# Kernel tuning notes

Hardware: AMD Instinct MI355X
Metric: run time of the kernel (lower is better)

The kernel has to match this reference:

```python
import jax, jax.numpy as jnp
import numpy as np

D_QK = 32  # out_channels // 8


def conv1x1(x, w, b):
    # x: [B,C,H,W], w: [O,C], b: [O] -> [B,O,H,W]
    return jnp.einsum('bchw,oc->bohw', x, w) + b[None, :, None, None]


def setup_inputs() -> dict:
    key = jax.random.key(0)
    ks = jax.random.split(key, 10)
    B, C, H, W = 4, 256, 64, 64
    in_ch, out_ch, attn_ch = 512, 256, 256
    s_in = 1.0 / np.sqrt(in_ch)
    s_at = 1.0 / np.sqrt(attn_ch)
    return {
        'ef': jax.random.normal(ks[0], (B, C, H, W), jnp.float32),
        'sf': jax.random.normal(ks[1], (B, C, H, W), jnp.float32),
        'Attn': jax.random.normal(ks[2], (B, attn_ch, H, W), jnp.float32),
        'Qw': jax.random.uniform(ks[3], (D_QK, in_ch), jnp.float32, -s_in, s_in),
        'Qb': jax.random.uniform(ks[4], (D_QK,), jnp.float32, -s_in, s_in),
        'Kw': jax.random.uniform(ks[5], (D_QK, attn_ch), jnp.float32, -s_at, s_at),
        'Kb': jax.random.uniform(ks[6], (D_QK,), jnp.float32, -s_at, s_at),
        'Vw': jax.random.uniform(ks[7], (out_ch, in_ch), jnp.float32, -s_in, s_in),
        'Vb': jax.random.uniform(ks[8], (out_ch,), jnp.float32, -s_in, s_in),
        'gamma': jnp.ones((1,), jnp.float32) * 0.25,
    }


def reference(ef, sf, Attn, Qw, Qb, Kw, Kb, Vw, Vb, gamma):
    B, C, H, W = ef.shape
    N = H * W
    x = jnp.concatenate((ef, sf), axis=1)  # [B, 2C, H, W]
    q = conv1x1(x, Qw, Qb).reshape(B, D_QK, N)         # [B, d, N]
    k = conv1x1(Attn, Kw, Kb).reshape(B, D_QK, N)      # [B, d, N]
    # scores[b, m, n] = sum_d q[b, d, m] * k[b, d, n]  (no 1/sqrt(d) scale)
    scores = jnp.einsum('bdm,bdn->bmn', q, k)
    attn = jax.nn.softmax(scores, axis=-1)             # [B, N, N]
    v = conv1x1(x, Vw, Vb).reshape(B, C, N)            # [B, C, N]
    # out[b, c, m] = sum_n v[b, c, n] * attn[b, m, n]
    out = jnp.einsum('bcn,bmn->bcm', v, attn).reshape(B, C, H, W)
    return gamma[0] * out + ef
```

## Files before the change

kernel.cpp:

```cpp
#include <hip/hip_runtime.h>
#include <hip/hip_bf16.h>

typedef short bf16x8 __attribute__((ext_vector_type(8)));
typedef float f32x4 __attribute__((ext_vector_type(4)));

#define MFMA16(a, b, c) __builtin_amdgcn_mfma_f32_16x16x32_bf16(a, b, c, 0, 0, 0)

#define NB 4
#define NC 256
#define NSP 4096

__device__ __forceinline__ unsigned short f2bf(float f) {
    return (unsigned short)((__float_as_uint(f) + 0x8000u) >> 16);
}
__device__ __forceinline__ unsigned pk2bf(float hi, float lo) {
    return __builtin_amdgcn_perm(__float_as_uint(hi) + 0x8000u,
                                 __float_as_uint(lo) + 0x8000u, 0x07060302u);
}

__global__ __launch_bounds__(256) void prep_w(
    const float* __restrict__ Qw, const float* __restrict__ Kw,
    const float* __restrict__ Vw,
    unsigned short* __restrict__ Qwbf, unsigned short* __restrict__ Kwbf,
    unsigned short* __restrict__ Vwbf)
{
    int i = blockIdx.x * 256 + threadIdx.x;
    {
        const float4* vs = (const float4*)(Vw + (size_t)i * 8);
        float4 a = vs[0], c = vs[1];
        int4 st;
        st.x = (int)pk2bf(a.y, a.x); st.y = (int)pk2bf(a.w, a.z);
        st.z = (int)pk2bf(c.y, c.x); st.w = (int)pk2bf(c.w, c.z);
        *(int4*)(Vwbf + (size_t)i * 8) = st;
    }
    if (i < 2048) {
        const float4* qs = (const float4*)(Qw + (size_t)i * 8);
        float4 a = qs[0], c = qs[1];
        int4 st;
        st.x = (int)pk2bf(a.y, a.x); st.y = (int)pk2bf(a.w, a.z);
        st.z = (int)pk2bf(c.y, c.x); st.w = (int)pk2bf(c.w, c.z);
        *(int4*)(Qwbf + (size_t)i * 8) = st;
    }
    if (i < 1024) {
        const float4* ks = (const float4*)(Kw + (size_t)i * 8);
        float4 a = ks[0], c = ks[1];
        int4 st;
        st.x = (int)pk2bf(a.y, a.x); st.y = (int)pk2bf(a.w, a.z);
        st.z = (int)pk2bf(c.y, c.x); st.w = (int)pk2bf(c.w, c.z);
        *(int4*)(Kwbf + (size_t)i * 8) = st;
    }
}

__global__ __launch_bounds__(256) void prep_x(
    const float* __restrict__ ef, const float* __restrict__ sf,
    const float* __restrict__ attn,
    unsigned short* __restrict__ xt, unsigned short* __restrict__ at)
{
    __shared__ float tile[64][65];
    int gid = blockIdx.x;
    const float* src; unsigned short* dst;
    int mt, cdst0, CW;
    if (gid < 2048) {
        int b = gid >> 9, r = gid & 511;
        mt = r >> 3; int ct = r & 7;
        src = (ct < 4 ? ef : sf) + ((size_t)(b * NC) + (ct & 3) * 64) * NSP;
        dst = xt + (size_t)b * NSP * 512; cdst0 = ct * 64; CW = 512;
    } else {
        int g2 = gid - 2048;
        int b = g2 >> 8, r = g2 & 255;
        mt = r >> 2; int ct = r & 3;
        src = attn + ((size_t)(b * NC) + ct * 64) * NSP;
        dst = at + (size_t)b * NSP * 256; cdst0 = ct * 64; CW = 256;
    }
    int m0 = mt * 64;
    int t = threadIdx.x;
    int ml = t & 63, cl = t >> 6;
#pragma unroll
    for (int r = 0; r < 16; ++r)
        tile[ml][r * 4 + cl] = src[(size_t)(r * 4 + cl) * NSP + m0 + ml];
    __syncthreads();
    int cp = t & 31, mw = t >> 5;
#pragma unroll
    for (int r = 0; r < 8; ++r) {
        int m_l = r * 8 + mw;
        float v0 = tile[m_l][2 * cp], v1 = tile[m_l][2 * cp + 1];
        *(unsigned*)(dst + (size_t)(m0 + m_l) * CW + cdst0 + 2 * cp) = pk2bf(v1, v0);
    }
}

__global__ __launch_bounds__(256) void proj_qk(
    const unsigned short* __restrict__ xt, const unsigned short* __restrict__ at,
    const unsigned short* __restrict__ Qwbf, const unsigned short* __restrict__ Kwbf,
    const float* __restrict__ Qb, const float* __restrict__ Kb,
    unsigned short* __restrict__ qws, unsigned short* __restrict__ kws)
{
    int t = threadIdx.x;
    int w = t >> 6, lane = t & 63, quad = lane >> 4, l15 = lane & 15;
    int b = blockIdx.x >> 6, m0 = (blockIdx.x & 63) * 64;
    int m = m0 + w * 16;

    f32x4 zero = {0.f, 0.f, 0.f, 0.f};
    f32x4 aq0 = zero, aq1 = zero, ak0 = zero, ak1 = zero;

    const unsigned short* xrow = xt + ((size_t)(b * NSP) + m + l15) * 512;
#pragma unroll
    for (int ks = 0; ks < 16; ++ks) {
        bf16x8 af = *(const bf16x8*)(xrow + ks * 32 + quad * 8);
        bf16x8 b0 = *(const bf16x8*)(Qwbf + (size_t)l15 * 512 + ks * 32 + quad * 8);
        bf16x8 b1 = *(const bf16x8*)(Qwbf + (size_t)(16 + l15) * 512 + ks * 32 + quad * 8);
        aq0 = MFMA16(af, b0, aq0);
        aq1 = MFMA16(af, b1, aq1);
    }
    const unsigned short* arow = at + ((size_t)(b * NSP) + m + l15) * 256;
#pragma unroll
    for (int ks = 0; ks < 8; ++ks) {
        bf16x8 af = *(const bf16x8*)(arow + ks * 32 + quad * 8);
        bf16x8 b0 = *(const bf16x8*)(Kwbf + (size_t)l15 * 256 + ks * 32 + quad * 8);
        bf16x8 b1 = *(const bf16x8*)(Kwbf + (size_t)(16 + l15) * 256 + ks * 32 + quad * 8);
        ak0 = MFMA16(af, b0, ak0);
        ak1 = MFMA16(af, b1, ak1);
    }
    float bq0 = Qb[l15], bq1 = Qb[16 + l15];
    float bk0 = Kb[l15], bk1 = Kb[16 + l15];
#pragma unroll
    for (int r = 0; r < 4; ++r) {
        size_t mr = (size_t)(b * NSP) + m + quad * 4 + r;
        qws[mr * 32 + l15]      = f2bf(aq0[r] + bq0);
        qws[mr * 32 + 16 + l15] = f2bf(aq1[r] + bq1);
        kws[mr * 32 + l15]      = f2bf(ak0[r] + bk0);
        kws[mr * 32 + 16 + l15] = f2bf(ak1[r] + bk1);
    }
}

__global__ __launch_bounds__(256) void proj_v(
    const unsigned short* __restrict__ xt,
    const unsigned short* __restrict__ Vwbf, const float* __restrict__ Vb,
    unsigned short* __restrict__ vws)
{
    int t = threadIdx.x;
    int w = t >> 6, lane = t & 63, quad = lane >> 4, l15 = lane & 15;
    int mt = blockIdx.x, coh = blockIdx.y, b = blockIdx.z;
    int m0 = mt * 32;
    int co0 = coh * 128 + w * 32;

    f32x4 zero = {0.f, 0.f, 0.f, 0.f};
    f32x4 acc[2][2];
    acc[0][0] = zero; acc[0][1] = zero; acc[1][0] = zero; acc[1][1] = zero;

    const unsigned short* x0 = xt + ((size_t)(b * NSP) + m0 + l15) * 512;
    const unsigned short* x1 = x0 + 16 * 512;
    const unsigned short* vw0 = Vwbf + (size_t)(co0 + l15) * 512;
    const unsigned short* vw1 = Vwbf + (size_t)(co0 + 16 + l15) * 512;
#pragma unroll
    for (int ks = 0; ks < 16; ++ks) {
        bf16x8 a0 = *(const bf16x8*)(x0 + ks * 32 + quad * 8);
        bf16x8 a1 = *(const bf16x8*)(x1 + ks * 32 + quad * 8);
        bf16x8 b0 = *(const bf16x8*)(vw0 + ks * 32 + quad * 8);
        bf16x8 b1 = *(const bf16x8*)(vw1 + ks * 32 + quad * 8);
        acc[0][0] = MFMA16(a0, b0, acc[0][0]);
        acc[0][1] = MFMA16(a0, b1, acc[0][1]);
        acc[1][0] = MFMA16(a1, b0, acc[1][0]);
        acc[1][1] = MFMA16(a1, b1, acc[1][1]);
    }
#pragma unroll
    for (int mi = 0; mi < 2; ++mi)
#pragma unroll
        for (int ci = 0; ci < 2; ++ci) {
            int co = co0 + ci * 16 + l15;
            float bias = Vb[co];
            unsigned short* vp = vws + ((size_t)(b * 128 + mt) * 256 + co) * 32;
#pragma unroll
            for (int r = 0; r < 4; ++r)
                vp[2 * (quad * 4 + r) + mi] = f2bf(acc[mi][ci][r] + bias);
        }
}

__global__ __launch_bounds__(512, 2) void attention(
    const unsigned short* __restrict__ qws, const unsigned short* __restrict__ kws,
    const unsigned short* __restrict__ vws, const float* __restrict__ ef,
    const float* __restrict__ gamma, float* __restrict__ out)
{
    __shared__ unsigned short Plds[2][2][64 * 40];
    __shared__ float mrg[256][68];
    __shared__ float denl[2][64];

    int t = threadIdx.x;
    int g = t >> 8, tl = t & 255;
    int w = tl >> 6, lane = tl & 63, quad = lane >> 4, l15 = lane & 15;
    int b = blockIdx.x >> 6, m0 = (blockIdx.x & 63) << 6;

    const unsigned short* kbase = kws + (size_t)(b * NSP) * 32;
    const unsigned short* vbase = vws + (size_t)(b * 128) * 8192;

    bf16x8 qf = *(const bf16x8*)(qws + ((size_t)(b * NSP) + m0 + w * 16 + l15) * 32 + quad * 8);

    f32x4 zero = {0.f, 0.f, 0.f, 0.f};
    f32x4 acc[4][4];
#pragma unroll
    for (int i = 0; i < 4; ++i)
#pragma unroll
        for (int j = 0; j < 4; ++j) acc[i][j] = zero;
    float lp0 = 0.f, lp1 = 0.f, lp2 = 0.f, lp3 = 0.f;

    int nt0 = g * 64;
    bf16x8 kf0 = *(const bf16x8*)(kbase + (size_t)(nt0 * 32 + l15) * 32 + quad * 8);
    bf16x8 kf1 = *(const bf16x8*)(kbase + (size_t)(nt0 * 32 + 16 + l15) * 32 + quad * 8);
    bf16x8 vf[4];
#pragma unroll
    for (int cc = 0; cc < 4; ++cc)
        vf[cc] = *(const bf16x8*)(vbase + (size_t)nt0 * 8192 + (w * 64 + cc * 16 + l15) * 32 + quad * 8);

    for (int it = 0; it < 64; ++it) {
        int buf = it & 1;
        f32x4 s0 = MFMA16(qf, kf0, zero);
        f32x4 s1 = MFMA16(qf, kf1, zero);
        float e00 = __expf(s0[0]), e01 = __expf(s0[1]), e02 = __expf(s0[2]), e03 = __expf(s0[3]);
        float e10 = __expf(s1[0]), e11 = __expf(s1[1]), e12 = __expf(s1[2]), e13 = __expf(s1[3]);
        lp0 += e00 + e10; lp1 += e01 + e11; lp2 += e02 + e12; lp3 += e03 + e13;

        {
            unsigned short* pb = &Plds[g][buf][(w * 16 + quad * 4) * 40 + 2 * l15];
            *(unsigned*)(pb)           = pk2bf(e10, e00);
            *(unsigned*)(pb + 40)      = pk2bf(e11, e01);
            *(unsigned*)(pb + 80)      = pk2bf(e12, e02);
            *(unsigned*)(pb + 120)     = pk2bf(e13, e03);
        }

        int itn = it + 1 < 64 ? it + 1 : 63;
        int ntn = nt0 + itn;
        kf0 = *(const bf16x8*)(kbase + (size_t)(ntn * 32 + l15) * 32 + quad * 8);
        kf1 = *(const bf16x8*)(kbase + (size_t)(ntn * 32 + 16 + l15) * 32 + quad * 8);
        bf16x8 vfn[4];
#pragma unroll
        for (int cc = 0; cc < 4; ++cc)
            vfn[cc] = *(const bf16x8*)(vbase + (size_t)ntn * 8192 + (w * 64 + cc * 16 + l15) * 32 + quad * 8);

        __syncthreads();

        bf16x8 pa0 = *(const bf16x8*)&Plds[g][buf][(0  + l15) * 40 + quad * 8];
        bf16x8 pa1 = *(const bf16x8*)&Plds[g][buf][(16 + l15) * 40 + quad * 8];
        bf16x8 pa2 = *(const bf16x8*)&Plds[g][buf][(32 + l15) * 40 + quad * 8];
        bf16x8 pa3 = *(const bf16x8*)&Plds[g][buf][(48 + l15) * 40 + quad * 8];
#pragma unroll
        for (int cc = 0; cc < 4; ++cc) {
            acc[0][cc] = MFMA16(pa0, vf[cc], acc[0][cc]);
            acc[1][cc] = MFMA16(pa1, vf[cc], acc[1][cc]);
            acc[2][cc] = MFMA16(pa2, vf[cc], acc[2][cc]);
            acc[3][cc] = MFMA16(pa3, vf[cc], acc[3][cc]);
        }
#pragma unroll
        for (int cc = 0; cc < 4; ++cc) vf[cc] = vfn[cc];
    }

    lp0 += __shfl_xor(lp0, 1); lp0 += __shfl_xor(lp0, 2); lp0 += __shfl_xor(lp0, 4); lp0 += __shfl_xor(lp0, 8);
    lp1 += __shfl_xor(lp1, 1); lp1 += __shfl_xor(lp1, 2); lp1 += __shfl_xor(lp1, 4); lp1 += __shfl_xor(lp1, 8);
    lp2 += __shfl_xor(lp2, 1); lp2 += __shfl_xor(lp2, 2); lp2 += __shfl_xor(lp2, 4); lp2 += __shfl_xor(lp2, 8);
    lp3 += __shfl_xor(lp3, 1); lp3 += __shfl_xor(lp3, 2); lp3 += __shfl_xor(lp3, 4); lp3 += __shfl_xor(lp3, 8);
    if (l15 == 0) {
        int base = w * 16 + quad * 4;
        denl[g][base + 0] = lp0; denl[g][base + 1] = lp1;
        denl[g][base + 2] = lp2; denl[g][base + 3] = lp3;
    }
    if (g == 1) {
#pragma unroll
        for (int qc = 0; qc < 4; ++qc)
#pragma unroll
            for (int cc = 0; cc < 4; ++cc)
                *(f32x4*)&mrg[w * 64 + cc * 16 + l15][qc * 16 + quad * 4] = acc[qc][cc];
    }
    __syncthreads();

    if (g == 0) {
        float gam = gamma[0];
#pragma unroll
        for (int qc = 0; qc < 4; ++qc) {
            int qb = qc * 16 + quad * 4;
            float4 d0 = *(const float4*)&denl[0][qb];
            float4 d1 = *(const float4*)&denl[1][qb];
            float r0 = gam / (d0.x + d1.x), r1 = gam / (d0.y + d1.y);
            float r2 = gam / (d0.z + d1.z), r3 = gam / (d0.w + d1.w);
#pragma unroll
            for (int cc = 0; cc < 4; ++cc) {
                int ch = w * 64 + cc * 16 + l15;
                f32x4 part = *(const f32x4*)&mrg[ch][qb];
                size_t off = ((size_t)(b * NC + ch)) * NSP + m0 + qb;
                float4 e = *(const float4*)(ef + off);
                float4 o;
                o.x = (acc[qc][cc][0] + part[0]) * r0 + e.x;
                o.y = (acc[qc][cc][1] + part[1]) * r1 + e.y;
                o.z = (acc[qc][cc][2] + part[2]) * r2 + e.z;
                o.w = (acc[qc][cc][3] + part[3]) * r3 + e.w;
                *(float4*)(out + off) = o;
            }
        }
    }
}

extern "C" void kernel_launch(void* const* d_in, const int* in_sizes, int n_in,
                              void* d_out, int out_size, void* d_ws, size_t ws_size,
                              hipStream_t stream) {
    const float* ef    = (const float*)d_in[0];
    const float* sf    = (const float*)d_in[1];
    const float* attn  = (const float*)d_in[2];
    const float* Qw    = (const float*)d_in[3];
    const float* Qb    = (const float*)d_in[4];
    const float* Kw    = (const float*)d_in[5];
    const float* Kb    = (const float*)d_in[6];
    const float* Vw    = (const float*)d_in[7];
    const float* Vb    = (const float*)d_in[8];
    const float* gamma = (const float*)d_in[9];
    float* out = (float*)d_out;

    unsigned short* qws  = (unsigned short*)d_ws;
    unsigned short* kws  = qws + (size_t)4 * 4096 * 32;
    unsigned short* vws  = kws + (size_t)4 * 4096 * 32;
    unsigned short* xt   = vws + (size_t)4 * 128 * 256 * 32;
    unsigned short* at   = xt  + (size_t)4 * 4096 * 512;
    unsigned short* Qwbf = at  + (size_t)4 * 4096 * 256;
    unsigned short* Kwbf = Qwbf + 32 * 512;
    unsigned short* Vwbf = Kwbf + 32 * 256;

    hipLaunchKernelGGL(prep_w, dim3(64), dim3(256), 0, stream,
                       Qw, Kw, Vw, Qwbf, Kwbf, Vwbf);
    hipLaunchKernelGGL(prep_x, dim3(3072), dim3(256), 0, stream,
                       ef, sf, attn, xt, at);
    hipLaunchKernelGGL(proj_qk, dim3(256), dim3(256), 0, stream,
                       xt, at, Qwbf, Kwbf, Qb, Kb, qws, kws);
    hipLaunchKernelGGL(proj_v, dim3(128, 2, 4), dim3(256), 0, stream,
                       xt, Vwbf, Vb, vws);
    hipLaunchKernelGGL(attention, dim3(256), dim3(512), 0, stream,
                       qws, kws, vws, ef, gamma, out);
}
```

Measured before the change: 202.4 us.

## Merge prep/projection kernels, fold log2e into Q, process two key tiles per step

Merges the weight and activation prep kernels into one launch, and the Q/K/V projections into a single launch, which cuts kernel-launch overhead and the gaps between kernels. Q is prescaled by log2(e) so the attention loop can call the hardware exp2 directly instead of __expf. The attention inner loop now handles two 32-key tiles per iteration, with a wider LDS P buffer, so it does half as many barriers and more MFMAs per sync. The cost is higher register pressure from double K/V prefetch fragments, and the extra bf16 rounding of the scaled Q can shift accuracy slightly.

```diff
diff --git a/kernel.cpp b/kernel.cpp
--- a/kernel.cpp
+++ b/kernel.cpp
@@ -9,6 +9,7 @@
 #define NB 4
 #define NC 256
 #define NSP 4096
+#define LOG2E 1.4426950408889634f
 
 __device__ __forceinline__ unsigned short f2bf(float f) {
     return (unsigned short)((__float_as_uint(f) + 0x8000u) >> 16);
@@ -18,46 +19,48 @@
                                  __float_as_uint(lo) + 0x8000u, 0x07060302u);
 }
 
-__global__ __launch_bounds__(256) void prep_w(
+__global__ __launch_bounds__(256) void prep(
+    const float* __restrict__ ef, const float* __restrict__ sf,
+    const float* __restrict__ attn,
     const float* __restrict__ Qw, const float* __restrict__ Kw,
     const float* __restrict__ Vw,
+    unsigned short* __restrict__ xt, unsigned short* __restrict__ at,
     unsigned short* __restrict__ Qwbf, unsigned short* __restrict__ Kwbf,
     unsigned short* __restrict__ Vwbf)
 {
-    int i = blockIdx.x * 256 + threadIdx.x;
-    {
-        const float4* vs = (const float4*)(Vw + (size_t)i * 8);
-        float4 a = vs[0], c = vs[1];
-        int4 st;
-        st.x = (int)pk2bf(a.y, a.x); st.y = (int)pk2bf(a.w, a.z);
-        st.z = (int)pk2bf(c.y, c.x); st.w = (int)pk2bf(c.w, c.z);
-        *(int4*)(Vwbf + (size_t)i * 8) = st;
-    }
-    if (i < 2048) {
-        const float4* qs = (const float4*)(Qw + (size_t)i * 8);
-        float4 a = qs[0], c = qs[1];
-        int4 st;
-        st.x = (int)pk2bf(a.y, a.x); st.y = (int)pk2bf(a.w, a.z);
-        st.z = (int)pk2bf(c.y, c.x); st.w = (int)pk2bf(c.w, c.z);
-        *(int4*)(Qwbf + (size_t)i * 8) = st;
-    }
-    if (i < 1024) {
-        const float4* ks = (const float4*)(Kw + (size_t)i * 8);
-        float4 a = ks[0], c = ks[1];
-        int4 st;
-        st.x = (int)pk2bf(a.y, a.x); st.y = (int)pk2bf(a.w, a.z);
-        st.z = (int)pk2bf(c.y, c.x); st.w = (int)pk2bf(c.w, c.z);
-        *(int4*)(Kwbf + (size_t)i * 8) = st;
-    }
-}
-
-__global__ __launch_bounds__(256) void prep_x(
-    const float* __restrict__ ef, const float* __restrict__ sf,
-    const float* __restrict__ attn,
-    unsigned short* __restrict__ xt, unsigned short* __restrict__ at)
-{
     __shared__ float tile[64][65];
     int gid = blockIdx.x;
+    int t = threadIdx.x;
+
+    if (gid >= 3072) {
+        int i = (gid - 3072) * 256 + t;
+        {
+            const float4* vs = (const float4*)(Vw + (size_t)i * 8);
+            float4 a = vs[0], c = vs[1];
+            int4 st;
+            st.x = (int)pk2bf(a.y, a.x); st.y = (int)pk2bf(a.w, a.z);
+            st.z = (int)pk2bf(c.y, c.x); st.w = (int)pk2bf(c.w, c.z);
+            *(int4*)(Vwbf + (size_t)i * 8) = st;
+        }
+        if (i < 2048) {
+            const float4* qs = (const float4*)(Qw + (size_t)i * 8);
+            float4 a = qs[0], c = qs[1];
+            int4 st;
+            st.x = (int)pk2bf(a.y, a.x); st.y = (int)pk2bf(a.w, a.z);
+            st.z = (int)pk2bf(c.y, c.x); st.w = (int)pk2bf(c.w, c.z);
+            *(int4*)(Qwbf + (size_t)i * 8) = st;
+        }
+        if (i < 1024) {
+            const float4* ks = (const float4*)(Kw + (size_t)i * 8);
+            float4 a = ks[0], c = ks[1];
+            int4 st;
+            st.x = (int)pk2bf(a.y, a.x); st.y = (int)pk2bf(a.w, a.z);
+            st.z = (int)pk2bf(c.y, c.x); st.w = (int)pk2bf(c.w, c.z);
+            *(int4*)(Kwbf + (size_t)i * 8) = st;
+        }
+        return;
+    }
+
     const float* src; unsigned short* dst;
     int mt, cdst0, CW;
     if (gid < 2048) {
@@ -73,7 +76,6 @@
         dst = at + (size_t)b * NSP * 256; cdst0 = ct * 64; CW = 256;
     }
     int m0 = mt * 64;
-    int t = threadIdx.x;
     int ml = t & 63, cl = t >> 6;
 #pragma unroll
     for (int r = 0; r < 16; ++r)
@@ -88,91 +90,95 @@
     }
 }
 
-__global__ __launch_bounds__(256) void proj_qk(
+__global__ __launch_bounds__(256, 4) void proj(
     const unsigned short* __restrict__ xt, const unsigned short* __restrict__ at,
     const unsigned short* __restrict__ Qwbf, const unsigned short* __restrict__ Kwbf,
+    const unsigned short* __restrict__ Vwbf,
     const float* __restrict__ Qb, const float* __restrict__ Kb,
-    unsigned short* __restrict__ qws, unsigned short* __restrict__ kws)
+    const float* __restrict__ Vb,
+    unsigned short* __restrict__ qws, unsigned short* __restrict__ kws,
+    unsigned short* __restrict__ vws)
 {
+    int bi = blockIdx.x;
     int t = threadIdx.x;
     int w = t >> 6, lane = t & 63, quad = lane >> 4, l15 = lane & 15;
-    int b = blockIdx.x >> 6, m0 = (blockIdx.x & 63) * 64;
-    int m = m0 + w * 16;
-
     f32x4 zero = {0.f, 0.f, 0.f, 0.f};
-    f32x4 aq0 = zero, aq1 = zero, ak0 = zero, ak1 = zero;
-
-    const unsigned short* xrow = xt + ((size_t)(b * NSP) + m + l15) * 512;
-#pragma unroll
-    for (int ks = 0; ks < 16; ++ks) {
-        bf16x8 af = *(const bf16x8*)(xrow + ks * 32 + quad * 8);
-        bf16x8 b0 = *(const bf16x8*)(Qwbf + (size_t)l15 * 512 + ks * 32 + quad * 8);
-        bf16x8 b1 = *(const bf16x8*)(Qwbf + (size_t)(16 + l15) * 512 + ks * 32 + quad * 8);
-        aq0 = MFMA16(af, b0, aq0);
-        aq1 = MFMA16(af, b1, aq1);
-    }
-    const unsigned short* arow = at + ((size_t)(b * NSP) + m + l15) * 256;
-#pragma unroll
-    for (int ks = 0; ks < 8; ++ks) {
-        bf16x8 af = *(const bf16x8*)(arow + ks * 32 + quad * 8);
-        bf16x8 b0 = *(const bf16x8*)(Kwbf + (size_t)l15 * 256 + ks * 32 + quad * 8);
-        bf16x8 b1 = *(const bf16x8*)(Kwbf + (size_t)(16 + l15) * 256 + ks * 32 + quad * 8);
-        ak0 = MFMA16(af, b0, ak0);
-        ak1 = MFMA16(af, b1, ak1);
-    }
-    float bq0 = Qb[l15], bq1 = Qb[16 + l15];
-    float bk0 = Kb[l15], bk1 = Kb[16 + l15];
-#pragma unroll
-    for (int r = 0; r < 4; ++r) {
-        size_t mr = (size_t)(b * NSP) + m + quad * 4 + r;
-        qws[mr * 32 + l15]      = f2bf(aq0[r] + bq0);
-        qws[mr * 32 + 16 + l15] = f2bf(aq1[r] + bq1);
-        kws[mr * 32 + l15]      = f2bf(ak0[r] + bk0);
-        kws[mr * 32 + 16 + l15] = f2bf(ak1[r] + bk1);
-    }
-}
-
-__global__ __launch_bounds__(256) void proj_v(
-    const unsigned short* __restrict__ xt,
-    const unsigned short* __restrict__ Vwbf, const float* __restrict__ Vb,
-    unsigned short* __restrict__ vws)
-{
-    int t = threadIdx.x;
-    int w = t >> 6, lane = t & 63, quad = lane >> 4, l15 = lane & 15;
-    int mt = blockIdx.x, coh = blockIdx.y, b = blockIdx.z;
-    int m0 = mt * 32;
-    int co0 = coh * 128 + w * 32;
-
-    f32x4 zero = {0.f, 0.f, 0.f, 0.f};
-    f32x4 acc[2][2];
-    acc[0][0] = zero; acc[0][1] = zero; acc[1][0] = zero; acc[1][1] = zero;
-
-    const unsigned short* x0 = xt + ((size_t)(b * NSP) + m0 + l15) * 512;
-    const unsigned short* x1 = x0 + 16 * 512;
-    const unsigned short* vw0 = Vwbf + (size_t)(co0 + l15) * 512;
-    const unsigned short* vw1 = Vwbf + (size_t)(co0 + 16 + l15) * 512;
-#pragma unroll
-    for (int ks = 0; ks < 16; ++ks) {
-        bf16x8 a0 = *(const bf16x8*)(x0 + ks * 32 + quad * 8);
-        bf16x8 a1 = *(const bf16x8*)(x1 + ks * 32 + quad * 8);
-        bf16x8 b0 = *(const bf16x8*)(vw0 + ks * 32 + quad * 8);
-        bf16x8 b1 = *(const bf16x8*)(vw1 + ks * 32 + quad * 8);
-        acc[0][0] = MFMA16(a0, b0, acc[0][0]);
-        acc[0][1] = MFMA16(a0, b1, acc[0][1]);
-        acc[1][0] = MFMA16(a1, b0, acc[1][0]);
-        acc[1][1] = MFMA16(a1, b1, acc[1][1]);
-    }
-#pragma unroll
-    for (int mi = 0; mi < 2; ++mi)
-#pragma unroll
-        for (int ci = 0; ci < 2; ++ci) {
-            int co = co0 + ci * 16 + l15;
-            float bias = Vb[co];
-            unsigned short* vp = vws + ((size_t)(b * 128 + mt) * 256 + co) * 32;
-#pragma unroll
-            for (int r = 0; r < 4; ++r)
-                vp[2 * (quad * 4 + r) + mi] = f2bf(acc[mi][ci][r] + bias);
-        }
+
+    if (bi < 256) {
+        int b = bi >> 6, m = (bi & 63) * 64 + w * 16;
+        f32x4 a0 = zero, a1 = zero;
+        const unsigned short* xrow = xt + ((size_t)(b * NSP) + m + l15) * 512;
+#pragma unroll 4
+        for (int ks = 0; ks < 16; ++ks) {
+            bf16x8 af = *(const bf16x8*)(xrow + ks * 32 + quad * 8);
+            bf16x8 b0 = *(const bf16x8*)(Qwbf + (size_t)l15 * 512 + ks * 32 + quad * 8);
+            bf16x8 b1 = *(const bf16x8*)(Qwbf + (size_t)(16 + l15) * 512 + ks * 32 + quad * 8);
+            a0 = MFMA16(af, b0, a0);
+            a1 = MFMA16(af, b1, a1);
+        }
+        float bq0 = Qb[l15], bq1 = Qb[16 + l15];
+#pragma unroll
+        for (int r = 0; r < 4; ++r) {
+            size_t mr = (size_t)(b * NSP) + m + quad * 4 + r;
+            qws[mr * 32 + l15]      = f2bf((a0[r] + bq0) * LOG2E);
+            qws[mr * 32 + 16 + l15] = f2bf((a1[r] + bq1) * LOG2E);
+        }
+    } else if (bi < 512) {
+        int r2 = bi - 256;
+        int b = r2 >> 6, m = (r2 & 63) * 64 + w * 16;
+        f32x4 a0 = zero, a1 = zero;
+        const unsigned short* arow = at + ((size_t)(b * NSP) + m + l15) * 256;
+#pragma unroll 4
+        for (int ks = 0; ks < 8; ++ks) {
+            bf16x8 af = *(const bf16x8*)(arow + ks * 32 + quad * 8);
+            bf16x8 b0 = *(const bf16x8*)(Kwbf + (size_t)l15 * 256 + ks * 32 + quad * 8);
+            bf16x8 b1 = *(const bf16x8*)(Kwbf + (size_t)(16 + l15) * 256 + ks * 32 + quad * 8);
+            a0 = MFMA16(af, b0, a0);
+            a1 = MFMA16(af, b1, a1);
+        }
+        float bk0 = Kb[l15], bk1 = Kb[16 + l15];
+#pragma unroll
+        for (int r = 0; r < 4; ++r) {
+            size_t mr = (size_t)(b * NSP) + m + quad * 4 + r;
+            kws[mr * 32 + l15]      = f2bf(a0[r] + bk0);
+            kws[mr * 32 + 16 + l15] = f2bf(a1[r] + bk1);
+        }
+    } else {
+        int r2 = bi - 512;
+        int mt = r2 & 127, coh = (r2 >> 7) & 1, b = r2 >> 8;
+        int m0 = mt * 32;
+        int co0 = coh * 128 + w * 32;
+
+        f32x4 acc[2][2];
+        acc[0][0] = zero; acc[0][1] = zero; acc[1][0] = zero; acc[1][1] = zero;
+
+        const unsigned short* x0 = xt + ((size_t)(b * NSP) + m0 + l15) * 512;
+        const unsigned short* x1 = x0 + 16 * 512;
+        const unsigned short* vw0 = Vwbf + (size_t)(co0 + l15) * 512;
+        const unsigned short* vw1 = Vwbf + (size_t)(co0 + 16 + l15) * 512;
+#pragma unroll 4
+        for (int ks = 0; ks < 16; ++ks) {
+            bf16x8 a0 = *(const bf16x8*)(x0 + ks * 32 + quad * 8);
+            bf16x8 a1 = *(const bf16x8*)(x1 + ks * 32 + quad * 8);
+            bf16x8 b0 = *(const bf16x8*)(vw0 + ks * 32 + quad * 8);
+            bf16x8 b1 = *(const bf16x8*)(vw1 + ks * 32 + quad * 8);
+            acc[0][0] = MFMA16(a0, b0, acc[0][0]);
+            acc[0][1] = MFMA16(a0, b1, acc[0][1]);
+            acc[1][0] = MFMA16(a1, b0, acc[1][0]);
+            acc[1][1] = MFMA16(a1, b1, acc[1][1]);
+        }
+#pragma unroll
+        for (int mi = 0; mi < 2; ++mi)
+#pragma unroll
+            for (int ci = 0; ci < 2; ++ci) {
+                int co = co0 + ci * 16 + l15;
+                float bias = Vb[co];
+                unsigned short* vp = vws + ((size_t)(b * 128 + mt) * 256 + co) * 32;
+#pragma unroll
+                for (int r = 0; r < 4; ++r)
+                    vp[2 * (quad * 4 + r) + mi] = f2bf(acc[mi][ci][r] + bias);
+            }
+    }
 }
 
 __global__ __launch_bounds__(512, 2) void attention(
@@ -180,7 +186,7 @@
     const unsigned short* __restrict__ vws, const float* __restrict__ ef,
     const float* __restrict__ gamma, float* __restrict__ out)
 {
-    __shared__ unsigned short Plds[2][2][64 * 40];
+    __shared__ unsigned short Plds[2][2][64 * 72];
     __shared__ float mrg[256][68];
     __shared__ float denl[2][64];
 
@@ -202,54 +208,77 @@
         for (int j = 0; j < 4; ++j) acc[i][j] = zero;
     float lp0 = 0.f, lp1 = 0.f, lp2 = 0.f, lp3 = 0.f;
 
-    int nt0 = g * 64;
-    bf16x8 kf0 = *(const bf16x8*)(kbase + (size_t)(nt0 * 32 + l15) * 32 + quad * 8);
-    bf16x8 kf1 = *(const bf16x8*)(kbase + (size_t)(nt0 * 32 + 16 + l15) * 32 + quad * 8);
-    bf16x8 vf[4];
-#pragma unroll
-    for (int cc = 0; cc < 4; ++cc)
-        vf[cc] = *(const bf16x8*)(vbase + (size_t)nt0 * 8192 + (w * 64 + cc * 16 + l15) * 32 + quad * 8);
-
-    for (int it = 0; it < 64; ++it) {
+    int tt0 = g * 64;
+    bf16x8 kf[4];
+#pragma unroll
+    for (int j = 0; j < 4; ++j)
+        kf[j] = *(const bf16x8*)(kbase + (size_t)((tt0 + (j >> 1)) * 32 + (j & 1) * 16 + l15) * 32 + quad * 8);
+    bf16x8 vf[2][4];
+#pragma unroll
+    for (int h = 0; h < 2; ++h)
+#pragma unroll
+        for (int cc = 0; cc < 4; ++cc)
+            vf[h][cc] = *(const bf16x8*)(vbase + (size_t)(tt0 + h) * 8192 + (w * 64 + cc * 16 + l15) * 32 + quad * 8);
+
+    for (int it = 0; it < 32; ++it) {
         int buf = it & 1;
-        f32x4 s0 = MFMA16(qf, kf0, zero);
-        f32x4 s1 = MFMA16(qf, kf1, zero);
-        float e00 = __expf(s0[0]), e01 = __expf(s0[1]), e02 = __expf(s0[2]), e03 = __expf(s0[3]);
-        float e10 = __expf(s1[0]), e11 = __expf(s1[1]), e12 = __expf(s1[2]), e13 = __expf(s1[3]);
-        lp0 += e00 + e10; lp1 += e01 + e11; lp2 += e02 + e12; lp3 += e03 + e13;
-
-        {
-            unsigned short* pb = &Plds[g][buf][(w * 16 + quad * 4) * 40 + 2 * l15];
-            *(unsigned*)(pb)           = pk2bf(e10, e00);
-            *(unsigned*)(pb + 40)      = pk2bf(e11, e01);
-            *(unsigned*)(pb + 80)      = pk2bf(e12, e02);
-            *(unsigned*)(pb + 120)     = pk2bf(e13, e03);
-        }
-
-        int itn = it + 1 < 64 ? it + 1 : 63;
-        int ntn = nt0 + itn;
-        kf0 = *(const bf16x8*)(kbase + (size_t)(ntn * 32 + l15) * 32 + quad * 8);
-        kf1 = *(const bf16x8*)(kbase + (size_t)(ntn * 32 + 16 + l15) * 32 + quad * 8);
-        bf16x8 vfn[4];
-#pragma unroll
-        for (int cc = 0; cc < 4; ++cc)
-            vfn[cc] = *(const bf16x8*)(vbase + (size_t)ntn * 8192 + (w * 64 + cc * 16 + l15) * 32 + quad * 8);
+        f32x4 s0 = MFMA16(qf, kf[0], zero);
+        f32x4 s1 = MFMA16(qf, kf[1], zero);
+        f32x4 s2 = MFMA16(qf, kf[2], zero);
+        f32x4 s3 = MFMA16(qf, kf[3], zero);
+
+        float e0[4], e1[4], e2[4], e3[4];
+#pragma unroll
+        for (int r = 0; r < 4; ++r) {
+            e0[r] = __builtin_amdgcn_exp2f(s0[r]);
+            e1[r] = __builtin_amdgcn_exp2f(s1[r]);
+            e2[r] = __builtin_amdgcn_exp2f(s2[r]);
+            e3[r] = __builtin_amdgcn_exp2f(s3[r]);
+        }
+        lp0 += (e0[0] + e1[0]) + (e2[0] + e3[0]);
+        lp1 += (e0[1] + e1[1]) + (e2[1] + e3[1]);
+        lp2 += (e0[2] + e1[2]) + (e2[2] + e3[2]);
+        lp3 += (e0[3] + e1[3]) + (e2[3] + e3[3]);
+
+        unsigned short* pd = &Plds[g][buf][(w * 16 + quad * 4) * 72 + 2 * l15];
+#pragma unroll
+        for (int r = 0; r < 4; ++r) {
+            *(unsigned*)(pd + r * 72)      = pk2bf(e1[r], e0[r]);
+            *(unsigned*)(pd + r * 72 + 32) = pk2bf(e3[r], e2[r]);
+        }
+
+        int itn = it + 1 < 32 ? it + 1 : 31;
+        int ttn = tt0 + 2 * itn;
+#pragma unroll
+        for (int j = 0; j < 4; ++j)
+            kf[j] = *(const bf16x8*)(kbase + (size_t)((ttn + (j >> 1)) * 32 + (j & 1) * 16 + l15) * 32 + quad * 8);
+        bf16x8 vfn[2][4];
+#pragma unroll
+        for (int h = 0; h < 2; ++h)
+#pragma unroll
+            for (int cc = 0; cc < 4; ++cc)
+                vfn[h][cc] = *(const bf16x8*)(vbase + (size_t)(ttn + h) * 8192 + (w * 64 + cc * 16 + l15) * 32 + quad * 8);
 
         __syncthreads();
 
-        bf16x8 pa0 = *(const bf16x8*)&Plds[g][buf][(0  + l15) * 40 + quad * 8];
-        bf16x8 pa1 = *(const bf16x8*)&Plds[g][buf][(16 + l15) * 40 + quad * 8];
-        bf16x8 pa2 = *(const bf16x8*)&Plds[g][buf][(32 + l15) * 40 + quad * 8];
-        bf16x8 pa3 = *(const bf16x8*)&Plds[g][buf][(48 + l15) * 40 + quad * 8];
-#pragma unroll
-        for (int cc = 0; cc < 4; ++cc) {
-            acc[0][cc] = MFMA16(pa0, vf[cc], acc[0][cc]);
-            acc[1][cc] = MFMA16(pa1, vf[cc], acc[1][cc]);
-            acc[2][cc] = MFMA16(pa2, vf[cc], acc[2][cc]);
-            acc[3][cc] = MFMA16(pa3, vf[cc], acc[3][cc]);
-        }
-#pragma unroll
-        for (int cc = 0; cc < 4; ++cc) vf[cc] = vfn[cc];
+#pragma unroll
+        for (int h = 0; h < 2; ++h) {
+            bf16x8 pa0 = *(const bf16x8*)&Plds[g][buf][(0  + l15) * 72 + h * 32 + quad * 8];
+            bf16x8 pa1 = *(const bf16x8*)&Plds[g][buf][(16 + l15) * 72 + h * 32 + quad * 8];
+            bf16x8 pa2 = *(const bf16x8*)&Plds[g][buf][(32 + l15) * 72 + h * 32 + quad * 8];
+            bf16x8 pa3 = *(const bf16x8*)&Plds[g][buf][(48 + l15) * 72 + h * 32 + quad * 8];
+#pragma unroll
+            for (int cc = 0; cc < 4; ++cc) {
+                acc[0][cc] = MFMA16(pa0, vf[h][cc], acc[0][cc]);
+                acc[1][cc] = MFMA16(pa1, vf[h][cc], acc[1][cc]);
+                acc[2][cc] = MFMA16(pa2, vf[h][cc], acc[2][cc]);
+                acc[3][cc] = MFMA16(pa3, vf[h][cc], acc[3][cc]);
+            }
+        }
+#pragma unroll
+        for (int h = 0; h < 2; ++h)
+#pragma unroll
+            for (int cc = 0; cc < 4; ++cc) vf[h][cc] = vfn[h][cc];
     }
 
     lp0 += __shfl_xor(lp0, 1); lp0 += __shfl_xor(lp0, 2); lp0 += __shfl_xor(lp0, 4); lp0 += __shfl_xor(lp0, 8);
@@ -320,14 +349,10 @@
     unsigned short* Kwbf = Qwbf + 32 * 512;
     unsigned short* Vwbf = Kwbf + 32 * 256;
 
-    hipLaunchKernelGGL(prep_w, dim3(64), dim3(256), 0, stream,
-                       Qw, Kw, Vw, Qwbf, Kwbf, Vwbf);
-    hipLaunchKernelGGL(prep_x, dim3(3072), dim3(256), 0, stream,
-                       ef, sf, attn, xt, at);
-    hipLaunchKernelGGL(proj_qk, dim3(256), dim3(256), 0, stream,
-                       xt, at, Qwbf, Kwbf, Qb, Kb, qws, kws);
-    hipLaunchKernelGGL(proj_v, dim3(128, 2, 4), dim3(256), 0, stream,
-                       xt, Vwbf, Vb, vws);
+    hipLaunchKernelGGL(prep, dim3(3136), dim3(256), 0, stream,
+                       ef, sf, attn, Qw, Kw, Vw, xt, at, Qwbf, Kwbf, Vwbf);
+    hipLaunchKernelGGL(proj, dim3(1536), dim3(256), 0, stream,
+                       xt, at, Qwbf, Kwbf, Vwbf, Qb, Kb, Vb, qws, kws, vws);
     hipLaunchKernelGGL(attention, dim3(256), dim3(512), 0, stream,
                        qws, kws, vws, ef, gamma, out);
 }
```

Result: faster. 198.0 us (-2.2%).
